# Performance work log

Measured on AMD Instinct MI355X. Metric: run time of the kernel, lower is better.

## Reference

```python
import jax, jax.numpy as jnp
import numpy as np

B, T, D = 4, 1024, 256
H, DK, C = 8, 32, 16  # n_heads, d_key, pos-encoder hidden units
DV = D // H
NEG = -1e15
EPS_SM = 1e-5
EPS_LN = 1e-5
SLOPE = 0.01  # LeakyReLU default


def setup_inputs() -> dict:
    key = jax.random.key(0)
    ks = jax.random.split(key, 16)
    s = 0.05
    x = jax.random.normal(ks[0], (B, T, D), jnp.float32)
    src_mask = jax.random.randint(ks[1], (B, T, T), 0, 2).astype(bool)
    rel_dists = jax.random.uniform(ks[2], (B, 1, T, T), jnp.float32)
    Wq = jax.random.normal(ks[3], (H, DK, D), jnp.float32) * s
    Wk = jax.random.normal(ks[4], (H, DK, D), jnp.float32) * s
    Wv = jax.random.normal(ks[5], (H, DV, D), jnp.float32) * s
    pw1 = jax.random.normal(ks[6], (H, C), jnp.float32) * s
    pb1 = jax.random.normal(ks[7], (H, C), jnp.float32) * s
    pw2 = jax.random.normal(ks[8], (H, C), jnp.float32) * s
    pb2 = jax.random.normal(ks[9], (H,), jnp.float32) * s
    Wo = jax.random.normal(ks[10], (D, D), jnp.float32) * s
    bo = jax.random.normal(ks[11], (D,), jnp.float32) * s
    Wf = jax.random.normal(ks[12], (D, D), jnp.float32) * s
    bf = jax.random.normal(ks[13], (D,), jnp.float32) * s
    g1 = jnp.ones((D,), jnp.float32)
    beta1 = jnp.zeros((D,), jnp.float32)
    g2 = jnp.ones((D,), jnp.float32)
    beta2 = jnp.zeros((D,), jnp.float32)
    return dict(x=x, src_mask=src_mask, rel_dists=rel_dists, Wq=Wq, Wk=Wk, Wv=Wv,
                pw1=pw1, pb1=pb1, pw2=pw2, pb2=pb2, Wo=Wo, bo=bo, Wf=Wf, bf=bf,
                g1=g1, beta1=beta1, g2=g2, beta2=beta2)


def _l2norm(v):
    # F.normalize(p=2, dim=-1): v / max(||v||, 1e-12)
    n = jnp.sqrt(jnp.sum(v * v, axis=-1, keepdims=True))
    return v / jnp.maximum(n, 1e-12)


def _lrelu(h):
    return jnp.where(h >= 0, h, SLOPE * h)


def _pos_bias(d, pw1, pb1, pw2, pb2):
    # d: [B,T,T]; per-head 1x1-conv MLP applied elementwise.
    # Loop over the tiny channel dim (16) to avoid a [B,H,T,T,C] intermediate.
    bias = jnp.broadcast_to(pb2[None, :, None, None], (d.shape[0], pw1.shape[0], d.shape[1], d.shape[2]))
    for c in range(pw1.shape[1]):
        h = d[:, None] * pw1[None, :, c, None, None] + pb1[None, :, c, None, None]
        bias = bias + pw2[None, :, c, None, None] * _lrelu(h)
    return bias  # [B,H,T,T]


def _layer_norm(v, g, b):
    mu = jnp.mean(v, axis=-1, keepdims=True)
    var = jnp.mean((v - mu) ** 2, axis=-1, keepdims=True)
    return (v - mu) * jax.lax.rsqrt(var + EPS_LN) * g + b


def reference(x, src_mask, rel_dists, Wq, Wk, Wv, pw1, pb1, pw2, pb2,
              Wo, bo, Wf, bf, g1, beta1, g2, beta2):
    # cosine-normalized multi-head attention (all heads batched)
    q = _l2norm(jnp.einsum('btd,hkd->bhtk', x, Wq))
    k = _l2norm(jnp.einsum('bsd,hkd->bhsk', x, Wk))
    v = jnp.einsum('bsd,hvd->bhsv', x, Wv)
    logits = jnp.einsum('bhtk,bhsk->bhts', q, k)
    logits = logits - _pos_bias(rel_dists[:, 0], pw1, pb1, pw2, pb2)
    logits = jnp.where(src_mask[:, None], NEG, logits)
    # custom softmax: exp / (sum + 1e-5) (handles all-padded rows)
    z = jnp.exp(logits)
    attn = z / (jnp.sum(z, axis=-1, keepdims=True) + EPS_SM)
    heads = jnp.einsum('bhts,bhsv->bhtv', attn, v)
    y = heads.transpose(0, 2, 1, 3).reshape(x.shape[0], x.shape[1], -1)  # concat heads
    y = y @ Wo.T + bo
    # residual + LN + FFN (dropout is identity in eval mode)
    zz = _layer_norm(x + y, g1, beta1)
    z_ff = _lrelu(zz @ Wf.T + bf)
    return _layer_norm(zz + z_ff, g2, beta2)
```

## Files before the change

### kernel.cpp

```cpp
#include <hip/hip_runtime.h>
#include <math.h>

#define Bc 4
#define Tc 1024
#define Dc 256
#define Hc 8
#define Cc 16
#define LUTN 256

typedef __attribute__((ext_vector_type(8))) short short8;
typedef __attribute__((ext_vector_type(4))) float f32x4;

__device__ __forceinline__ unsigned bf16u(float x) {
    unsigned u = __float_as_uint(x);
    return (u + 0x7FFFu + ((u >> 16) & 1u)) >> 16;
}
__device__ __forceinline__ unsigned pk2(float lo, float hi) {
    return bf16u(lo) | (bf16u(hi) << 16);
}
__device__ __forceinline__ unsigned pk2t(float lo, float hi) {
    return __builtin_amdgcn_perm(__float_as_uint(hi), __float_as_uint(lo), 0x07060302u);
}
__device__ __forceinline__ unsigned pk2r(float lo, float hi) {
    unsigned a = __float_as_uint(lo) + 0x8000u;
    unsigned b = __float_as_uint(hi) + 0x8000u;
    return __builtin_amdgcn_perm(b, a, 0x07060302u);
}
__device__ __forceinline__ float upk(unsigned v) { return __uint_as_float(v << 16); }
__device__ __forceinline__ float upkh(unsigned v) { return __uint_as_float(v & 0xffff0000u); }

__device__ __forceinline__ short8 ld_cast8(const float* p) {
    float4 a = *(const float4*)p;
    float4 b = *(const float4*)(p + 4);
    union { uint4 u; short8 s; } c;
    c.u.x = pk2r(a.x, a.y); c.u.y = pk2r(a.z, a.w);
    c.u.z = pk2r(b.x, b.y); c.u.w = pk2r(b.z, b.w);
    return c.s;
}

__global__ __launch_bounds__(256) void qkv_direct(
    const float* __restrict__ x,
    const float* __restrict__ Wq, const float* __restrict__ Wk,
    const float* __restrict__ Wv,
    ushort* __restrict__ Qb, ushort* __restrict__ Kb, ushort* __restrict__ Vt)
{
    const int tid = threadIdx.x;
    const int w = tid >> 6;
    const int l = tid & 63;
    const int u = l & 15, g = l >> 4;
    const int rbase = blockIdx.x * 16;
    const int cb = (blockIdx.y * 4 + w) * 64;
    const int mat = cb >> 8;
    const int fcb = cb & 255;
    const float* Wsel = (mat == 0) ? Wq : (mat == 1) ? Wk : Wv;

    f32x4 acc[4];
#pragma unroll
    for (int nt = 0; nt < 4; ++nt) acc[nt] = (f32x4){0.f, 0.f, 0.f, 0.f};

    const float* arow = x + (size_t)(rbase + u) * 256 + g * 8;
#pragma unroll 2
    for (int k0 = 0; k0 < 256; k0 += 32) {
        short8 af = ld_cast8(arow + k0);
#pragma unroll
        for (int nt = 0; nt < 4; ++nt) {
            short8 bfr = ld_cast8(Wsel + (size_t)(fcb + nt * 16 + u) * 256 + k0 + g * 8);
            acc[nt] = __builtin_amdgcn_mfma_f32_16x16x32_bf16(af, bfr, acc[nt], 0, 0, 0);
        }
    }

    if (mat < 2) {
        ushort* Out = (mat == 0) ? Qb : Kb;
#pragma unroll
        for (int hp = 0; hp < 2; ++hp) {
            const int head = (fcb >> 5) + hp;
#pragma unroll
            for (int reg = 0; reg < 4; ++reg) {
                float ss = acc[2 * hp][reg] * acc[2 * hp][reg]
                         + acc[2 * hp + 1][reg] * acc[2 * hp + 1][reg];
                ss += __shfl_xor(ss, 1, 64);
                ss += __shfl_xor(ss, 2, 64);
                ss += __shfl_xor(ss, 4, 64);
                ss += __shfl_xor(ss, 8, 64);
                float scn = 1.f / fmaxf(sqrtf(ss), 1e-12f);
                const int t = rbase + 4 * g + reg;
                const int bb = t >> 10, tt = t & 1023;
                const size_t base = ((size_t)(bb * 8 + head) * Tc + tt) * 32;
                Out[base + u]      = (ushort)bf16u(acc[2 * hp][reg] * scn);
                Out[base + 16 + u] = (ushort)bf16u(acc[2 * hp + 1][reg] * scn);
            }
        }
    } else {
#pragma unroll
        for (int nt = 0; nt < 4; ++nt) {
            const int head = (fcb >> 5) + (nt >> 1);
            const int vt = nt & 1;
#pragma unroll
            for (int reg = 0; reg < 4; ++reg) {
                const int s = rbase + 4 * g + reg;
                const int bb = s >> 10, ss = s & 1023;
                const int bh = bb * 8 + head;
                Vt[(((size_t)bh * 32 + (ss >> 5)) * 2 + vt) * 512 + u * 32 + (ss & 31)] =
                    (ushort)bf16u(acc[nt][reg]);
            }
        }
    }
}

__global__ __launch_bounds__(256) void attn_mfma(
    const ushort* __restrict__ Qb, const ushort* __restrict__ Kb,
    const ushort* __restrict__ Vt,
    const float* __restrict__ rel, const int* __restrict__ msk,
    const float* __restrict__ pw1, const float* __restrict__ pb1,
    const float* __restrict__ pw2, const float* __restrict__ pb2,
    ushort* __restrict__ Yb)
{
    const int tid = threadIdx.x;
    const int w = tid >> 6;
    const int l = tid & 63;
    const int u = l & 15;
    const int g = l >> 4;
    const int t0 = blockIdx.x * 16;
    const int b = blockIdx.y;
    const int hg = blockIdx.z;

    __shared__ __align__(16) unsigned lut_su[LUTN * 2];
    __shared__ __align__(16) unsigned plds[4 * 320];
    __shared__ __align__(16) ushort comb[4 * 16 * 68];
    __shared__ float rs_s[4 * 2 * 16];

    {
        const int bin = tid;
        const float d0 = bin * (1.f / LUTN), d1 = (bin + 1) * (1.f / LUTN);
#pragma unroll
        for (int hp = 0; hp < 2; ++hp) {
            const int h = hg * 2 + hp;
            float y0 = pb2[h], y1 = pb2[h];
#pragma unroll
            for (int c = 0; c < Cc; ++c) {
                float w1 = pw1[h * Cc + c], b1 = pb1[h * Cc + c], w2 = pw2[h * Cc + c];
                float h0 = fmaf(w1, d0, b1), h1 = fmaf(w1, d1, b1);
                y0 = fmaf(w2, h0 >= 0.f ? h0 : 0.01f * h0, y0);
                y1 = fmaf(w2, h1 >= 0.f ? h1 : 0.01f * h1, y1);
            }
            float a = (y1 - y0) * (float)LUTN;
            lut_su[bin * 2 + hp] = pk2(a, y0 - a * d0);
        }
    }

    const int bh0 = b * 8 + hg * 2;
    short8 qf[2];
#pragma unroll
    for (int hi = 0; hi < 2; ++hi)
        qf[hi] = *(const short8*)(Qb + (((size_t)(bh0 + hi) * Tc + t0 + u) * 32 + g * 8));

    const short8 ones = (short8){0x3F80, 0x3F80, 0x3F80, 0x3F80,
                                 0x3F80, 0x3F80, 0x3F80, 0x3F80};

    f32x4 oacc[2][2];
    f32x4 rsacc[2];
#pragma unroll
    for (int hi = 0; hi < 2; ++hi) {
        oacc[hi][0] = (f32x4){0.f, 0.f, 0.f, 0.f};
        oacc[hi][1] = (f32x4){0.f, 0.f, 0.f, 0.f};
        rsacc[hi]   = (f32x4){0.f, 0.f, 0.f, 0.f};
    }

    unsigned* pwb = plds + w * 320;
    const size_t dbase = (size_t)b * Tc * Tc;

    __syncthreads();

    const int s_begin = w * 256;
    for (int sc = s_begin; sc < s_begin + 256; sc += 32) {
        float dA[4], dB[4];
#pragma unroll
        for (int reg = 0; reg < 4; ++reg) {
            const int t = t0 + 4 * g + reg;
            const size_t off = dbase + (size_t)t * Tc + sc + 2 * u;
            float2 d2 = *(const float2*)(rel + off);
            int2 m2 = *(const int2*)(msk + off);
            dA[reg] = m2.x ? -1.f : d2.x;
            dB[reg] = m2.y ? -1.f : d2.y;
        }
        float biasA[4][2], biasB[4][2];
#pragma unroll
        for (int reg = 0; reg < 4; ++reg) {
            int iA = (int)(dA[reg] * (float)LUTN);
            int iB = (int)(dB[reg] * (float)LUTN);
            iA = iA < 0 ? 0 : (iA > LUTN - 1 ? LUTN - 1 : iA);
            iB = iB < 0 ? 0 : (iB > LUTN - 1 ? LUTN - 1 : iB);
            uint2 wA = *(const uint2*)&lut_su[iA * 2];
            uint2 wB = *(const uint2*)&lut_su[iB * 2];
            biasA[reg][0] = fmaf(upk(wA.x), dA[reg], upkh(wA.x));
            biasA[reg][1] = fmaf(upk(wA.y), dA[reg], upkh(wA.y));
            biasB[reg][0] = fmaf(upk(wB.x), dB[reg], upkh(wB.x));
            biasB[reg][1] = fmaf(upk(wB.y), dB[reg], upkh(wB.y));
        }
#pragma unroll
        for (int hi = 0; hi < 2; ++hi) {
            const size_t kb = ((size_t)(bh0 + hi) * Tc + sc + 2 * u) * 32 + g * 8;
            short8 kfA = *(const short8*)(Kb + kb);
            short8 kfB = *(const short8*)(Kb + kb + 32);
            const f32x4 z4 = (f32x4){0.f, 0.f, 0.f, 0.f};
            f32x4 sA = __builtin_amdgcn_mfma_f32_16x16x32_bf16(qf[hi], kfA, z4, 0, 0, 0);
            f32x4 sB = __builtin_amdgcn_mfma_f32_16x16x32_bf16(qf[hi], kfB, z4, 0, 0, 0);
#pragma unroll
            for (int reg = 0; reg < 4; ++reg) {
                float zA = (dA[reg] < 0.f) ? 0.f : __expf(sA[reg] - biasA[reg][hi]);
                float zB = (dB[reg] < 0.f) ? 0.f : __expf(sB[reg] - biasB[reg][hi]);
                pwb[(4 * g + reg) * 20 + u] = pk2t(zA, zB);
            }
            short8 pf = *(const short8*)((const char*)pwb + u * 80 + g * 16);
            const ushort* vb = Vt + ((size_t)(bh0 + hi) * 32 + (sc >> 5)) * 1024;
            short8 vf0 = *(const short8*)(vb + u * 32 + g * 8);
            short8 vf1 = *(const short8*)(vb + 512 + u * 32 + g * 8);
            oacc[hi][0] = __builtin_amdgcn_mfma_f32_16x16x32_bf16(pf, vf0, oacc[hi][0], 0, 0, 0);
            oacc[hi][1] = __builtin_amdgcn_mfma_f32_16x16x32_bf16(pf, vf1, oacc[hi][1], 0, 0, 0);
            rsacc[hi]   = __builtin_amdgcn_mfma_f32_16x16x32_bf16(pf, ones, rsacc[hi], 0, 0, 0);
        }
    }

#pragma unroll
    for (int hi = 0; hi < 2; ++hi)
        if (u == 0) {
#pragma unroll
            for (int reg = 0; reg < 4; ++reg)
                rs_s[(w * 2 + hi) * 16 + 4 * g + reg] = rsacc[hi][reg];
        }
#pragma unroll
    for (int hi = 0; hi < 2; ++hi)
#pragma unroll
        for (int vt = 0; vt < 2; ++vt)
#pragma unroll
            for (int reg = 0; reg < 4; ++reg)
                comb[w * 1088 + (4 * g + reg) * 68 + hi * 32 + vt * 16 + u] =
                    (ushort)(__float_as_uint(oacc[hi][vt][reg]) >> 16);
    __syncthreads();

    const int tl = tid >> 4;
    const int c4 = (tid & 15) * 4;
    const int hl = c4 >> 5;
    float rstot = rs_s[(0 + hl) * 16 + tl] + rs_s[(2 + hl) * 16 + tl]
                + rs_s[(4 + hl) * 16 + tl] + rs_s[(6 + hl) * 16 + tl];
    float inv = 1.f / (rstot + 1e-5f);
    float o[4] = {0.f, 0.f, 0.f, 0.f};
#pragma unroll
    for (int ww = 0; ww < 4; ++ww) {
        uint2 pv = *(const uint2*)&comb[ww * 1088 + tl * 68 + c4];
        o[0] += upk(pv.x); o[1] += upkh(pv.x);
        o[2] += upk(pv.y); o[3] += upkh(pv.y);
    }
    uint2 pw;
    pw.x = pk2(o[0] * inv, o[1] * inv);
    pw.y = pk2(o[2] * inv, o[3] * inv);
    *(uint2*)(Yb + ((size_t)b * Tc + t0 + tl) * Dc + hg * 64 + c4) = pw;
}

__global__ __launch_bounds__(256) void proj_ffn_ln(
    const ushort* __restrict__ Yb,
    const float* __restrict__ Wo, const float* __restrict__ bo,
    const float* __restrict__ x,
    const float* __restrict__ g1, const float* __restrict__ be1,
    const float* __restrict__ Wf, const float* __restrict__ bf,
    const float* __restrict__ g2, const float* __restrict__ be2,
    float* __restrict__ out)
{
    const int tid = threadIdx.x;
    const int w = tid >> 6;
    const int l = tid & 63;
    const int u = l & 15, g = l >> 4;
    const int rbase = blockIdx.x * 16;

    __shared__ float red1[64], red2[64], red3[64], red4[64];
    __shared__ __align__(16) ushort zz[16][264];

    f32x4 acc[4];
#pragma unroll
    for (int nt = 0; nt < 4; ++nt) acc[nt] = (f32x4){0.f, 0.f, 0.f, 0.f};
    const ushort* arow = Yb + (size_t)(rbase + u) * 256 + g * 8;
#pragma unroll 2
    for (int k0 = 0; k0 < 256; k0 += 32) {
        short8 af = *(const short8*)(arow + k0);
#pragma unroll
        for (int nt = 0; nt < 4; ++nt) {
            short8 bfr = ld_cast8(Wo + (size_t)(w * 64 + nt * 16 + u) * 256 + k0 + g * 8);
            acc[nt] = __builtin_amdgcn_mfma_f32_16x16x32_bf16(af, bfr, acc[nt], 0, 0, 0);
        }
    }

    float sv[4][4];
#pragma unroll
    for (int reg = 0; reg < 4; ++reg) {
        const int row = rbase + 4 * g + reg;
        float s1 = 0.f, s2 = 0.f;
#pragma unroll
        for (int nt = 0; nt < 4; ++nt) {
            const int col = w * 64 + nt * 16 + u;
            float v = acc[nt][reg] + bo[col];
            float s = v + x[(size_t)row * 256 + col];
            sv[reg][nt] = s;
            s1 += s;
            s2 = fmaf(s, s, s2);
        }
        s1 += __shfl_xor(s1, 1, 64); s2 += __shfl_xor(s2, 1, 64);
        s1 += __shfl_xor(s1, 2, 64); s2 += __shfl_xor(s2, 2, 64);
        s1 += __shfl_xor(s1, 4, 64); s2 += __shfl_xor(s2, 4, 64);
        s1 += __shfl_xor(s1, 8, 64); s2 += __shfl_xor(s2, 8, 64);
        if (u == 0) { red1[w * 16 + 4 * g + reg] = s1; red2[w * 16 + 4 * g + reg] = s2; }
    }
    __syncthreads();

    float zzv[4][4];
#pragma unroll
    for (int reg = 0; reg < 4; ++reg) {
        const int rl = 4 * g + reg;
        float S1 = red1[rl] + red1[16 + rl] + red1[32 + rl] + red1[48 + rl];
        float S2 = red2[rl] + red2[16 + rl] + red2[32 + rl] + red2[48 + rl];
        float mu = S1 * (1.f / 256.f);
        float var = S2 * (1.f / 256.f) - mu * mu;
        float rsig = rsqrtf(var + 1e-5f);
#pragma unroll
        for (int nt = 0; nt < 4; ++nt) {
            const int col = w * 64 + nt * 16 + u;
            float o = (sv[reg][nt] - mu) * rsig * g1[col] + be1[col];
            zzv[reg][nt] = o;
            zz[rl][col] = (ushort)bf16u(o);
        }
    }
    __syncthreads();

    f32x4 acc2[4];
#pragma unroll
    for (int nt = 0; nt < 4; ++nt) acc2[nt] = (f32x4){0.f, 0.f, 0.f, 0.f};
#pragma unroll 2
    for (int k0 = 0; k0 < 256; k0 += 32) {
        short8 af = *(const short8*)&zz[u][k0 + g * 8];
#pragma unroll
        for (int nt = 0; nt < 4; ++nt) {
            short8 bfr = ld_cast8(Wf + (size_t)(w * 64 + nt * 16 + u) * 256 + k0 + g * 8);
            acc2[nt] = __builtin_amdgcn_mfma_f32_16x16x32_bf16(af, bfr, acc2[nt], 0, 0, 0);
        }
    }

    float s2v[4][4];
#pragma unroll
    for (int reg = 0; reg < 4; ++reg) {
        float s1 = 0.f, s2 = 0.f;
#pragma unroll
        for (int nt = 0; nt < 4; ++nt) {
            const int col = w * 64 + nt * 16 + u;
            float v = acc2[nt][reg] + bf[col];
            v = v >= 0.f ? v : 0.01f * v;
            float s = v + zzv[reg][nt];
            s2v[reg][nt] = s;
            s1 += s;
            s2 = fmaf(s, s, s2);
        }
        s1 += __shfl_xor(s1, 1, 64); s2 += __shfl_xor(s2, 1, 64);
        s1 += __shfl_xor(s1, 2, 64); s2 += __shfl_xor(s2, 2, 64);
        s1 += __shfl_xor(s1, 4, 64); s2 += __shfl_xor(s2, 4, 64);
        s1 += __shfl_xor(s1, 8, 64); s2 += __shfl_xor(s2, 8, 64);
        if (u == 0) { red3[w * 16 + 4 * g + reg] = s1; red4[w * 16 + 4 * g + reg] = s2; }
    }
    __syncthreads();

#pragma unroll
    for (int reg = 0; reg < 4; ++reg) {
        const int row = rbase + 4 * g + reg;
        const int rl = 4 * g + reg;
        float S1 = red3[rl] + red3[16 + rl] + red3[32 + rl] + red3[48 + rl];
        float S2 = red4[rl] + red4[16 + rl] + red4[32 + rl] + red4[48 + rl];
        float mu = S1 * (1.f / 256.f);
        float var = S2 * (1.f / 256.f) - mu * mu;
        float rsig = rsqrtf(var + 1e-5f);
#pragma unroll
        for (int nt = 0; nt < 4; ++nt) {
            const int col = w * 64 + nt * 16 + u;
            out[(size_t)row * 256 + col] = (s2v[reg][nt] - mu) * rsig * g2[col] + be2[col];
        }
    }
}

extern "C" void kernel_launch(void* const* d_in, const int* in_sizes, int n_in,
                              void* d_out, int out_size, void* d_ws, size_t ws_size,
                              hipStream_t stream) {
    const float* x    = (const float*)d_in[0];
    const int*   mask = (const int*)d_in[1];
    const float* rel  = (const float*)d_in[2];
    const float* Wq   = (const float*)d_in[3];
    const float* Wk   = (const float*)d_in[4];
    const float* Wv   = (const float*)d_in[5];
    const float* pw1  = (const float*)d_in[6];
    const float* pb1  = (const float*)d_in[7];
    const float* pw2  = (const float*)d_in[8];
    const float* pb2  = (const float*)d_in[9];
    const float* Wo   = (const float*)d_in[10];
    const float* bo   = (const float*)d_in[11];
    const float* Wf   = (const float*)d_in[12];
    const float* bf   = (const float*)d_in[13];
    const float* g1   = (const float*)d_in[14];
    const float* be1  = (const float*)d_in[15];
    const float* g2   = (const float*)d_in[16];
    const float* be2  = (const float*)d_in[17];
    float* out = (float*)d_out;

    char* wsb = (char*)d_ws;
    ushort* Qb = (ushort*)(wsb);
    ushort* Kb = (ushort*)(wsb + (size_t)(2 << 20));
    ushort* Vt = (ushort*)(wsb + (size_t)(4 << 20));
    ushort* Yb = (ushort*)(wsb + (size_t)(6 << 20));

    qkv_direct<<<dim3(256, 3), 256, 0, stream>>>(x, Wq, Wk, Wv, Qb, Kb, Vt);
    attn_mfma<<<dim3(64, 4, 4), 256, 0, stream>>>(Qb, Kb, Vt, rel, mask,
                                                  pw1, pb1, pw2, pb2, Yb);
    proj_ffn_ln<<<256, 256, 0, stream>>>(Yb, Wo, bo, x, g1, be1,
                                         Wf, bf, g2, be2, out);
}
```

Baseline: 192.7 us.

## Precompute bf16 masked distances and process four heads per attention block

A new prep kernel fuses rel_dists and the mask into one bf16 array and builds the per-head bias LUT once, scaled by log2(e). The attention kernel now handles four heads per block instead of two, so each distance read is shared by more heads, and it uses exp2 with log2(e) folded into Q. The aim is to cut the repeated fp32 rel/mask traffic (8 bytes per element read by every head group) down to one compact read. The trade-offs are an extra kernel pass over the full T×T data, half as many attention blocks, and higher register pressure from the larger per-head accumulators. Rounding the distances to bf16 also changes bias precision slightly.

```diff
diff --git a/kernel.cpp b/kernel.cpp
--- a/kernel.cpp
+++ b/kernel.cpp
@@ -7,6 +7,7 @@
 #define Hc 8
 #define Cc 16
 #define LUTN 256
+#define LOG2E 1.4426950408889634f
 
 typedef __attribute__((ext_vector_type(8))) short short8;
 typedef __attribute__((ext_vector_type(4))) float f32x4;
@@ -28,6 +29,7 @@
 }
 __device__ __forceinline__ float upk(unsigned v) { return __uint_as_float(v << 16); }
 __device__ __forceinline__ float upkh(unsigned v) { return __uint_as_float(v & 0xffff0000u); }
+__device__ __forceinline__ float fexp2(float x) { return __builtin_amdgcn_exp2f(x); }
 
 __device__ __forceinline__ short8 ld_cast8(const float* p) {
     float4 a = *(const float4*)p;
@@ -36,6 +38,44 @@
     c.u.x = pk2r(a.x, a.y); c.u.y = pk2r(a.z, a.w);
     c.u.z = pk2r(b.x, b.y); c.u.w = pk2r(b.z, b.w);
     return c.s;
+}
+
+__global__ __launch_bounds__(256) void prep(
+    const float* __restrict__ rel, const int* __restrict__ msk,
+    const float* __restrict__ pw1, const float* __restrict__ pb1,
+    const float* __restrict__ pw2, const float* __restrict__ pb2,
+    ushort* __restrict__ Dm, ushort* __restrict__ LUTb)
+{
+    if (blockIdx.x == 2048) {
+        const int bin = threadIdx.x;
+        const float d0 = bin * (1.f / LUTN), d1 = (bin + 1) * (1.f / LUTN);
+        for (int h = 0; h < Hc; ++h) {
+            float y0 = pb2[h], y1 = pb2[h];
+#pragma unroll
+            for (int c = 0; c < Cc; ++c) {
+                float w1 = pw1[h * Cc + c], b1 = pb1[h * Cc + c], w2 = pw2[h * Cc + c];
+                float h0 = fmaf(w1, d0, b1), h1 = fmaf(w1, d1, b1);
+                y0 = fmaf(w2, h0 >= 0.f ? h0 : 0.01f * h0, y0);
+                y1 = fmaf(w2, h1 >= 0.f ? h1 : 0.01f * h1, y1);
+            }
+            float a = (y1 - y0) * (float)LUTN;
+            float b = y0 - a * d0;
+            LUTb[(h >> 2) * 2048 + bin * 8 + (h & 3) * 2]     = (ushort)bf16u(a * LOG2E);
+            LUTb[(h >> 2) * 2048 + bin * 8 + (h & 3) * 2 + 1] = (ushort)bf16u(b * LOG2E);
+        }
+        return;
+    }
+    const size_t e = ((size_t)blockIdx.x * 256 + threadIdx.x) * 8;
+    float4 d0 = *(const float4*)(rel + e);
+    float4 d1 = *(const float4*)(rel + e + 4);
+    int4 m0 = *(const int4*)(msk + e);
+    int4 m1 = *(const int4*)(msk + e + 4);
+    uint4 o;
+    o.x = pk2(m0.x ? -1.f : d0.x, m0.y ? -1.f : d0.y);
+    o.y = pk2(m0.z ? -1.f : d0.z, m0.w ? -1.f : d0.w);
+    o.z = pk2(m1.x ? -1.f : d1.x, m1.y ? -1.f : d1.y);
+    o.w = pk2(m1.z ? -1.f : d1.z, m1.w ? -1.f : d1.w);
+    *(uint4*)(Dm + e) = o;
 }
 
 __global__ __launch_bounds__(256) void qkv_direct(
@@ -71,6 +111,7 @@
 
     if (mat < 2) {
         ushort* Out = (mat == 0) ? Qb : Kb;
+        const float post = (mat == 0) ? LOG2E : 1.f;
 #pragma unroll
         for (int hp = 0; hp < 2; ++hp) {
             const int head = (fcb >> 5) + hp;
@@ -82,7 +123,7 @@
                 ss += __shfl_xor(ss, 2, 64);
                 ss += __shfl_xor(ss, 4, 64);
                 ss += __shfl_xor(ss, 8, 64);
-                float scn = 1.f / fmaxf(sqrtf(ss), 1e-12f);
+                float scn = post / fmaxf(sqrtf(ss), 1e-12f);
                 const int t = rbase + 4 * g + reg;
                 const int bb = t >> 10, tt = t & 1023;
                 const size_t base = ((size_t)(bb * 8 + head) * Tc + tt) * 32;
@@ -110,9 +151,7 @@
 __global__ __launch_bounds__(256) void attn_mfma(
     const ushort* __restrict__ Qb, const ushort* __restrict__ Kb,
     const ushort* __restrict__ Vt,
-    const float* __restrict__ rel, const int* __restrict__ msk,
-    const float* __restrict__ pw1, const float* __restrict__ pb1,
-    const float* __restrict__ pw2, const float* __restrict__ pb2,
+    const ushort* __restrict__ Dm, const ushort* __restrict__ LUTb,
     ushort* __restrict__ Yb)
 {
     const int tid = threadIdx.x;
@@ -124,43 +163,26 @@
     const int b = blockIdx.y;
     const int hg = blockIdx.z;
 
-    __shared__ __align__(16) unsigned lut_su[LUTN * 2];
+    __shared__ __align__(16) ushort lut_s[2048];
     __shared__ __align__(16) unsigned plds[4 * 320];
-    __shared__ __align__(16) ushort comb[4 * 16 * 68];
-    __shared__ float rs_s[4 * 2 * 16];
-
-    {
-        const int bin = tid;
-        const float d0 = bin * (1.f / LUTN), d1 = (bin + 1) * (1.f / LUTN);
-#pragma unroll
-        for (int hp = 0; hp < 2; ++hp) {
-            const int h = hg * 2 + hp;
-            float y0 = pb2[h], y1 = pb2[h];
-#pragma unroll
-            for (int c = 0; c < Cc; ++c) {
-                float w1 = pw1[h * Cc + c], b1 = pb1[h * Cc + c], w2 = pw2[h * Cc + c];
-                float h0 = fmaf(w1, d0, b1), h1 = fmaf(w1, d1, b1);
-                y0 = fmaf(w2, h0 >= 0.f ? h0 : 0.01f * h0, y0);
-                y1 = fmaf(w2, h1 >= 0.f ? h1 : 0.01f * h1, y1);
-            }
-            float a = (y1 - y0) * (float)LUTN;
-            lut_su[bin * 2 + hp] = pk2(a, y0 - a * d0);
-        }
-    }
-
-    const int bh0 = b * 8 + hg * 2;
-    short8 qf[2];
-#pragma unroll
-    for (int hi = 0; hi < 2; ++hi)
+    __shared__ __align__(16) ushort comb[4 * 16 * 136];
+    __shared__ float rs_s[4 * 64];
+
+    *(uint4*)(lut_s + tid * 8) = *(const uint4*)(LUTb + hg * 2048 + tid * 8);
+
+    const int bh0 = b * 8 + hg * 4;
+    short8 qf[4];
+#pragma unroll
+    for (int hi = 0; hi < 4; ++hi)
         qf[hi] = *(const short8*)(Qb + (((size_t)(bh0 + hi) * Tc + t0 + u) * 32 + g * 8));
 
     const short8 ones = (short8){0x3F80, 0x3F80, 0x3F80, 0x3F80,
                                  0x3F80, 0x3F80, 0x3F80, 0x3F80};
 
-    f32x4 oacc[2][2];
-    f32x4 rsacc[2];
-#pragma unroll
-    for (int hi = 0; hi < 2; ++hi) {
+    f32x4 oacc[4][2];
+    f32x4 rsacc[4];
+#pragma unroll
+    for (int hi = 0; hi < 4; ++hi) {
         oacc[hi][0] = (f32x4){0.f, 0.f, 0.f, 0.f};
         oacc[hi][1] = (f32x4){0.f, 0.f, 0.f, 0.f};
         rsacc[hi]   = (f32x4){0.f, 0.f, 0.f, 0.f};
@@ -177,28 +199,30 @@
 #pragma unroll
         for (int reg = 0; reg < 4; ++reg) {
             const int t = t0 + 4 * g + reg;
-            const size_t off = dbase + (size_t)t * Tc + sc + 2 * u;
-            float2 d2 = *(const float2*)(rel + off);
-            int2 m2 = *(const int2*)(msk + off);
-            dA[reg] = m2.x ? -1.f : d2.x;
-            dB[reg] = m2.y ? -1.f : d2.y;
-        }
-        float biasA[4][2], biasB[4][2];
+            unsigned dm = *(const unsigned*)(Dm + dbase + (size_t)t * Tc + sc + 2 * u);
+            dA[reg] = upk(dm);
+            dB[reg] = upkh(dm);
+        }
+        float biasA[4][4], biasB[4][4];
 #pragma unroll
         for (int reg = 0; reg < 4; ++reg) {
             int iA = (int)(dA[reg] * (float)LUTN);
             int iB = (int)(dB[reg] * (float)LUTN);
             iA = iA < 0 ? 0 : (iA > LUTN - 1 ? LUTN - 1 : iA);
             iB = iB < 0 ? 0 : (iB > LUTN - 1 ? LUTN - 1 : iB);
-            uint2 wA = *(const uint2*)&lut_su[iA * 2];
-            uint2 wB = *(const uint2*)&lut_su[iB * 2];
+            uint4 wA = *(const uint4*)(lut_s + iA * 8);
+            uint4 wB = *(const uint4*)(lut_s + iB * 8);
             biasA[reg][0] = fmaf(upk(wA.x), dA[reg], upkh(wA.x));
             biasA[reg][1] = fmaf(upk(wA.y), dA[reg], upkh(wA.y));
+            biasA[reg][2] = fmaf(upk(wA.z), dA[reg], upkh(wA.z));
+            biasA[reg][3] = fmaf(upk(wA.w), dA[reg], upkh(wA.w));
             biasB[reg][0] = fmaf(upk(wB.x), dB[reg], upkh(wB.x));
             biasB[reg][1] = fmaf(upk(wB.y), dB[reg], upkh(wB.y));
-        }
-#pragma unroll
-        for (int hi = 0; hi < 2; ++hi) {
+            biasB[reg][2] = fmaf(upk(wB.z), dB[reg], upkh(wB.z));
+            biasB[reg][3] = fmaf(upk(wB.w), dB[reg], upkh(wB.w));
+        }
+#pragma unroll
+        for (int hi = 0; hi < 4; ++hi) {
             const size_t kb = ((size_t)(bh0 + hi) * Tc + sc + 2 * u) * 32 + g * 8;
             short8 kfA = *(const short8*)(Kb + kb);
             short8 kfB = *(const short8*)(Kb + kb + 32);
@@ -207,8 +231,8 @@
             f32x4 sB = __builtin_amdgcn_mfma_f32_16x16x32_bf16(qf[hi], kfB, z4, 0, 0, 0);
 #pragma unroll
             for (int reg = 0; reg < 4; ++reg) {
-                float zA = (dA[reg] < 0.f) ? 0.f : __expf(sA[reg] - biasA[reg][hi]);
-                float zB = (dB[reg] < 0.f) ? 0.f : __expf(sB[reg] - biasB[reg][hi]);
+                float zA = (dA[reg] < 0.f) ? 0.f : fexp2(sA[reg] - biasA[reg][hi]);
+                float zB = (dB[reg] < 0.f) ? 0.f : fexp2(sB[reg] - biasB[reg][hi]);
                 pwb[(4 * g + reg) * 20 + u] = pk2t(zA, zB);
             }
             short8 pf = *(const short8*)((const char*)pwb + u * 80 + g * 16);
@@ -222,39 +246,43 @@
     }
 
 #pragma unroll
-    for (int hi = 0; hi < 2; ++hi)
+    for (int hi = 0; hi < 4; ++hi)
         if (u == 0) {
 #pragma unroll
             for (int reg = 0; reg < 4; ++reg)
-                rs_s[(w * 2 + hi) * 16 + 4 * g + reg] = rsacc[hi][reg];
-        }
-#pragma unroll
-    for (int hi = 0; hi < 2; ++hi)
+                rs_s[(w * 4 + hi) * 16 + 4 * g + reg] = rsacc[hi][reg];
+        }
+#pragma unroll
+    for (int hi = 0; hi < 4; ++hi)
 #pragma unroll
         for (int vt = 0; vt < 2; ++vt)
 #pragma unroll
             for (int reg = 0; reg < 4; ++reg)
-                comb[w * 1088 + (4 * g + reg) * 68 + hi * 32 + vt * 16 + u] =
+                comb[w * 2176 + (4 * g + reg) * 136 + hi * 32 + vt * 16 + u] =
                     (ushort)(__float_as_uint(oacc[hi][vt][reg]) >> 16);
     __syncthreads();
 
     const int tl = tid >> 4;
-    const int c4 = (tid & 15) * 4;
-    const int hl = c4 >> 5;
-    float rstot = rs_s[(0 + hl) * 16 + tl] + rs_s[(2 + hl) * 16 + tl]
-                + rs_s[(4 + hl) * 16 + tl] + rs_s[(6 + hl) * 16 + tl];
+    const int f0 = (tid & 15) * 8;
+    const int hl = f0 >> 5;
+    float rstot = rs_s[(0 + hl) * 16 + tl] + rs_s[(4 + hl) * 16 + tl]
+                + rs_s[(8 + hl) * 16 + tl] + rs_s[(12 + hl) * 16 + tl];
     float inv = 1.f / (rstot + 1e-5f);
-    float o[4] = {0.f, 0.f, 0.f, 0.f};
+    float o[8];
+#pragma unroll
+    for (int k = 0; k < 8; ++k) o[k] = 0.f;
 #pragma unroll
     for (int ww = 0; ww < 4; ++ww) {
-        uint2 pv = *(const uint2*)&comb[ww * 1088 + tl * 68 + c4];
+        uint4 pv = *(const uint4*)&comb[ww * 2176 + tl * 136 + f0];
         o[0] += upk(pv.x); o[1] += upkh(pv.x);
         o[2] += upk(pv.y); o[3] += upkh(pv.y);
-    }
-    uint2 pw;
-    pw.x = pk2(o[0] * inv, o[1] * inv);
-    pw.y = pk2(o[2] * inv, o[3] * inv);
-    *(uint2*)(Yb + ((size_t)b * Tc + t0 + tl) * Dc + hg * 64 + c4) = pw;
+        o[4] += upk(pv.z); o[5] += upkh(pv.z);
+        o[6] += upk(pv.w); o[7] += upkh(pv.w);
+    }
+    uint4 pw;
+    pw.x = pk2(o[0] * inv, o[1] * inv); pw.y = pk2(o[2] * inv, o[3] * inv);
+    pw.z = pk2(o[4] * inv, o[5] * inv); pw.w = pk2(o[6] * inv, o[7] * inv);
+    *(uint4*)(Yb + ((size_t)b * Tc + t0 + tl) * Dc + hg * 128 + f0) = pw;
 }
 
 __global__ __launch_bounds__(256) void proj_ffn_ln(
@@ -406,14 +434,16 @@
     float* out = (float*)d_out;
 
     char* wsb = (char*)d_ws;
-    ushort* Qb = (ushort*)(wsb);
-    ushort* Kb = (ushort*)(wsb + (size_t)(2 << 20));
-    ushort* Vt = (ushort*)(wsb + (size_t)(4 << 20));
-    ushort* Yb = (ushort*)(wsb + (size_t)(6 << 20));
-
+    ushort* Qb   = (ushort*)(wsb);
+    ushort* Kb   = (ushort*)(wsb + (size_t)( 2 << 20));
+    ushort* Vt   = (ushort*)(wsb + (size_t)( 4 << 20));
+    ushort* Yb   = (ushort*)(wsb + (size_t)( 6 << 20));
+    ushort* Dm   = (ushort*)(wsb + (size_t)( 8 << 20));
+    ushort* LUTb = (ushort*)(wsb + (size_t)(16 << 20));
+
+    prep<<<2049, 256, 0, stream>>>(rel, mask, pw1, pb1, pw2, pb2, Dm, LUTb);
     qkv_direct<<<dim3(256, 3), 256, 0, stream>>>(x, Wq, Wk, Wv, Qb, Kb, Vt);
-    attn_mfma<<<dim3(64, 4, 4), 256, 0, stream>>>(Qb, Kb, Vt, rel, mask,
-                                                  pw1, pb1, pw2, pb2, Yb);
+    attn_mfma<<<dim3(64, 4, 2), 256, 0, stream>>>(Qb, Kb, Vt, Dm, LUTb, Yb);
     proj_ffn_ln<<<256, 256, 0, stream>>>(Yb, Wo, bo, x, g1, be1,
                                          Wf, bf, g2, be2, out);
 }
```

New measurement: 192.4 us. No clear change (-0.2%).
